# Optimization experiments

Hardware: AMD Instinct MI355X
Metric: run time of the kernel (lower is better)

## Reference

```python
import jax, jax.numpy as jnp
import numpy as np

D_MODEL = 2048
HEADS = 16
D_K = D_MODEL // HEADS  # 128
BATCH = 4
SEQ = 2048


def setup_inputs() -> dict:
    key = jax.random.key(0)
    ks = jax.random.split(key, 5)
    scale = (2.0 / (D_MODEL + D_MODEL)) ** 0.5  # trunc-normal std from init
    return {
        "x": jax.random.normal(ks[0], (BATCH, SEQ, D_MODEL), dtype=jnp.float32),
        "W_Q": jax.random.normal(ks[1], (D_MODEL, D_MODEL), dtype=jnp.float32) * scale,
        "W_K": jax.random.normal(ks[2], (D_MODEL, D_MODEL), dtype=jnp.float32) * scale,
        "W_V": jax.random.normal(ks[3], (D_MODEL, D_MODEL), dtype=jnp.float32) * scale,
        "W_O": jax.random.normal(ks[4], (D_MODEL, D_MODEL), dtype=jnp.float32) * scale,
    }


def reference(x, W_Q, W_K, W_V, W_O):
    b, s, d = x.shape
    # weights stored as [(h d_k), d_model] -> [h, d_k, d_model]
    wq = W_Q.reshape(HEADS, D_K, d)
    wk = W_K.reshape(HEADS, D_K, d)
    wv = W_V.reshape(HEADS, D_K, d)
    # projections: [b, h, s, d_k]
    Q = jnp.einsum("hkd,bsd->bhsk", wq, x)
    K = jnp.einsum("hkd,bsd->bhsk", wk, x)
    V = jnp.einsum("hvd,bsd->bhsv", wv, x)
    # causal scaled dot-product attention
    scores = jnp.einsum("bhqk,bhsk->bhqs", Q, K) / jnp.sqrt(jnp.asarray(D_K, x.dtype))
    causal = jnp.tril(jnp.ones((s, s), dtype=bool))  # True -> attend
    scores = jnp.where(causal, scores, jnp.asarray(-jnp.inf, x.dtype))
    attn = jax.nn.softmax(scores, axis=-1)
    mh = jnp.einsum("bhqs,bhsv->bhqv", attn, V)  # [b, h, s, d_v]
    # concat heads -> [b, s, h*d_v]
    mh = jnp.transpose(mh, (0, 2, 1, 3)).reshape(b, s, HEADS * D_K)
    # output projection: W_O is [d_model, (h d_v)]
    out = jnp.einsum("dm,bsm->bsd", W_O, mh)
    return out
```

## Files before the change

kernel.cpp:

```cpp
#include <hip/hip_runtime.h>
#include <stdint.h>

#define D_MODEL 2048
#define HEADS   16
#define DKH     128
#define BATCH   4
#define SEQ     2048
#define MROWS   (BATCH*SEQ)

typedef unsigned short u16;
typedef __attribute__((ext_vector_type(8))) short   short8;
typedef __attribute__((ext_vector_type(4))) float   floatx4;

#define Q_PRESCALE 0.12751744509914576f

__device__ __forceinline__ u16 f2bf(float f) {
  unsigned u = __float_as_uint(f);
  u += 0x7fffu + ((u >> 16) & 1u);
  return (u16)(u >> 16);
}
__device__ __forceinline__ u16 f2bf_fast(float f) {
  return (u16)((__float_as_uint(f) + 0x8000u) >> 16);
}

__device__ __forceinline__ void async_lds16(const u16* g, u16* l) {
  __builtin_amdgcn_global_load_lds(
      (const __attribute__((address_space(1))) unsigned int*)g,
      (__attribute__((address_space(3))) unsigned int*)l, 16, 0, 0);
}

__global__ void cast_all(const float4* __restrict__ x,  const float4* __restrict__ wq,
                         const float4* __restrict__ wk, const float4* __restrict__ wv,
                         const float4* __restrict__ wo, ushort4* __restrict__ dst) {
  int i = blockIdx.x * blockDim.x + threadIdx.x;
  int stride = gridDim.x * blockDim.x;
  for (; i < 8388608; i += stride) {
    const float4* s; int j;
    if (i < 4194304) { s = x; j = i; }
    else {
      int t = i - 4194304; int w = t >> 20; j = t & 1048575;
      s = (w == 0) ? wq : (w == 1) ? wk : (w == 2) ? wv : wo;
    }
    float4 f = s[j];
    ushort4 o;
    o.x = f2bf(f.x); o.y = f2bf(f.y); o.z = f2bf(f.z); o.w = f2bf(f.w);
    dst[i] = o;
  }
}

#define KDIM 2048
#define NKT  32

#define STAGE_A(t, buf) do { \
    const size_t go = (size_t)(t) * 64; \
    const int bo = (buf) * 32768; \
    async_lds16(sA0 + go,          dL0 + bo); \
    async_lds16(sA1 + go,          dL1 + bo); \
    async_lds16(sA0 + go + 262144, dL0 + bo + 8192); \
    async_lds16(sA1 + go + 262144, dL1 + bo + 8192); \
  } while (0)
#define STAGE_B(t, buf) do { \
    const size_t go = (size_t)(t) * 64; \
    const int bo = (buf) * 32768; \
    async_lds16(sB0 + go,          dL0 + bo + 16384); \
    async_lds16(sB1 + go,          dL1 + bo + 16384); \
    async_lds16(sB0 + go + 262144, dL0 + bo + 24576); \
    async_lds16(sB1 + go + 262144, dL1 + bo + 24576); \
  } while (0)

__device__ __forceinline__ void gemm256_core(
    const u16* __restrict__ A, const u16* __restrict__ B,
    u16* __restrict__ S, int rowBase, int colBase, floatx4 acc[8][4])
{
  const int tid  = threadIdx.x;
  const int lane = tid & 63;
  const int w    = tid >> 6;
  const int wm   = w >> 2, wn = w & 3;
  const int c    = lane & 15, quad = lane >> 4;

  const u16 *sA0, *sA1, *sB0, *sB1;
  {
    int L0 = tid * 16, L1 = 8192 + tid * 16;
    int Ls0 = L0 ^ (((L0 >> 7) & 7) << 4);
    int Ls1 = L1 ^ (((L1 >> 7) & 7) << 4);
    sA0 = A + (size_t)(rowBase + (Ls0 >> 7)) * KDIM + ((Ls0 & 127) >> 1);
    sA1 = A + (size_t)(rowBase + (Ls1 >> 7)) * KDIM + ((Ls1 & 127) >> 1);
    sB0 = B + (size_t)(colBase + (Ls0 >> 7)) * KDIM + ((Ls0 & 127) >> 1);
    sB1 = B + (size_t)(colBase + (Ls1 >> 7)) * KDIM + ((Ls1 & 127) >> 1);
  }
  u16* dL0 = S + tid * 8;
  u16* dL1 = S + 4096 + tid * 8;

  const int fo0 = (c * 128 + ((       quad * 16) ^ ((c & 7) << 4))) >> 1;
  const int fo1 = (c * 128 + ((64 +   quad * 16) ^ ((c & 7) << 4))) >> 1;
  const u16* aW = S + wm * 8192;
  const u16* bW = S + 16384 + (wn >> 1) * 8192 + (wn & 1) * 4096;

  const floatx4 z4 = {0.f, 0.f, 0.f, 0.f};
#pragma unroll
  for (int i = 0; i < 8; i++)
#pragma unroll
    for (int j = 0; j < 4; j++) acc[i][j] = z4;

  STAGE_A(0, 0); STAGE_B(0, 0);
  STAGE_A(1, 1); STAGE_B(1, 1);
  asm volatile("s_waitcnt vmcnt(8)" ::: "memory");
  __builtin_amdgcn_s_barrier();

  short8 aX[4][2], aY[4][2], bf[4][2];

#pragma unroll
  for (int i = 0; i < 4; i++) {
    aX[i][0] = *(const short8*)(aW + i * 1024 + fo0);
    aX[i][1] = *(const short8*)(aW + i * 1024 + fo1);
  }

  for (int t = 0; t < NKT; ++t) {
    const int b = t & 1;
    const u16* aB = aW + b * 32768;
    const u16* bB = bW + b * 32768;

#pragma unroll
    for (int j = 0; j < 4; j++) {
      bf[j][0] = *(const short8*)(bB + j * 1024 + fo0);
      bf[j][1] = *(const short8*)(bB + j * 1024 + fo1);
    }
#pragma unroll
    for (int i = 0; i < 4; i++) {
      aY[i][0] = *(const short8*)(aB + (4 + i) * 1024 + fo0);
      aY[i][1] = *(const short8*)(aB + (4 + i) * 1024 + fo1);
    }

    asm volatile("s_waitcnt lgkmcnt(8)" ::: "memory");
    __builtin_amdgcn_sched_barrier(0);
    __builtin_amdgcn_s_setprio(1);
#pragma unroll
    for (int i = 0; i < 4; i++)
#pragma unroll
      for (int j = 0; j < 4; j++) {
        acc[i][j] = __builtin_amdgcn_mfma_f32_16x16x32_bf16(aX[i][0], bf[j][0], acc[i][j], 0, 0, 0);
        acc[i][j] = __builtin_amdgcn_mfma_f32_16x16x32_bf16(aX[i][1], bf[j][1], acc[i][j], 0, 0, 0);
      }
    __builtin_amdgcn_s_setprio(0);

    asm volatile("s_waitcnt lgkmcnt(0)" ::: "memory");
    asm volatile("s_waitcnt vmcnt(0)" ::: "memory");
    __builtin_amdgcn_s_barrier();

    if (t + 2 < NKT) { STAGE_A(t + 2, b); STAGE_B(t + 2, b); }

    if (t + 1 < NKT) {
      const u16* aN = aW + (b ^ 1) * 32768;
#pragma unroll
      for (int i = 0; i < 4; i++) {
        aX[i][0] = *(const short8*)(aN + i * 1024 + fo0);
        aX[i][1] = *(const short8*)(aN + i * 1024 + fo1);
      }
    }
    __builtin_amdgcn_sched_barrier(0);
    __builtin_amdgcn_s_setprio(1);
#pragma unroll
    for (int i = 0; i < 4; i++)
#pragma unroll
      for (int j = 0; j < 4; j++) {
        acc[4 + i][j] = __builtin_amdgcn_mfma_f32_16x16x32_bf16(aY[i][0], bf[j][0], acc[4 + i][j], 0, 0, 0);
        acc[4 + i][j] = __builtin_amdgcn_mfma_f32_16x16x32_bf16(aY[i][1], bf[j][1], acc[4 + i][j], 0, 0, 0);
      }
    __builtin_amdgcn_s_setprio(0);
  }
}

__global__ __launch_bounds__(512, 2) void gemm_qkv(
    const u16* __restrict__ A, const u16* __restrict__ B,
    u16* __restrict__ Qb, u16* __restrict__ Kb, u16* __restrict__ Vpb)
{
  __shared__ __align__(16) u16 S[65536];

  const int tid  = threadIdx.x;
  const int lane = tid & 63;
  const int w    = tid >> 6;
  const int wm   = w >> 2, wn = w & 3;
  const int c    = lane & 15, quad = lane >> 4;
  const int rowBase = blockIdx.x * 256;
  const int colBase = blockIdx.y * 256;

  floatx4 acc[8][4];
  gemm256_core(A, B, S, rowBase, colBase, acc);

  const int proj = colBase >> 11;
  const float esc = (proj == 0) ? Q_PRESCALE : 1.0f;
  u16* dst = (proj == 0) ? Qb : (proj == 1) ? Kb : Vpb;

#pragma unroll
  for (int i = 0; i < 8; i++) {
#pragma unroll
    for (int j = 0; j < 4; j++) {
#pragma unroll
      for (int r = 0; r < 4; r++) {
        int row = rowBase + wm * 128 + i * 16 + quad * 4 + r;
        int col = (colBase & 2047) + wn * 64 + j * 16 + c;
        float v = acc[i][j][r] * esc;
        if (proj < 2) {
          size_t idx = ((size_t)((row >> 11) * HEADS + (col >> 7)) * SEQ + (row & 2047)) * DKH + (col & 127);
          dst[idx] = f2bf(v);
        } else {
          int srow = row & 2047;
          int sp = (srow & ~127) | (((srow & 15) << 3) | ((srow >> 4) & 7));
          size_t idx = ((size_t)((row >> 11) * HEADS + (col >> 7)) * DKH + (col & 127)) * SEQ + sp;
          dst[idx] = f2bf(v);
        }
      }
    }
  }
}

__global__ __launch_bounds__(512, 2) void gemm_out(
    const u16* __restrict__ A, const u16* __restrict__ B,
    float* __restrict__ Cout)
{
  __shared__ __align__(16) u16 S[65536];

  const int tid  = threadIdx.x;
  const int lane = tid & 63;
  const int w    = tid >> 6;
  const int wm   = w >> 2, wn = w & 3;
  const int c    = lane & 15, quad = lane >> 4;
  const int rowBase = blockIdx.x * 256;
  const int colBase = blockIdx.y * 256;

  floatx4 acc[8][4];
  gemm256_core(A, B, S, rowBase, colBase, acc);

#pragma unroll
  for (int i = 0; i < 8; i++)
#pragma unroll
    for (int j = 0; j < 4; j++)
#pragma unroll
      for (int r = 0; r < 4; r++) {
        int row = rowBase + wm * 128 + i * 16 + quad * 4 + r;
        int col = colBase + wn * 64 + j * 16 + c;
        Cout[(size_t)row * D_MODEL + col] = acc[i][j][r];
      }
}

__global__ __launch_bounds__(256, 1) void attn_fwd(
    const u16* __restrict__ Qg, const u16* __restrict__ Kg,
    const u16* __restrict__ Vpg, u16* __restrict__ mh)
{
  __shared__ __align__(16) u16 Sh[2 * 16384 + 16384 + 4 * 32 * 136];

  const int tid  = threadIdx.x;
  const int lane = tid & 63;
  const int w    = tid >> 6;
  const int c    = lane & 15, quad = lane >> 4;
  const int bh   = blockIdx.x;
  const int qt   = 15 - blockIdx.y;
  const int q0   = qt * 128;

  const u16* Qbh = Qg  + (size_t)bh * SEQ * DKH;
  const u16* Kbh = Kg  + (size_t)bh * SEQ * DKH;
  const u16* Vbh = Vpg + (size_t)bh * DKH * SEQ;

  u16* Vs = Sh + 32768;
  u16* Pw = Sh + 49152 + w * 32 * 136;

  const int rowb = tid >> 4;
  const int cbh  = (((tid & 15) ^ (rowb & 7)) << 3);
  const u16* sK = Kbh + rowb * DKH + cbh;
  const u16* sV = Vbh + (size_t)rowb * SEQ + cbh;

  int fof[4];
#pragma unroll
  for (int ks = 0; ks < 4; ks++)
    fof[ks] = ((ks * 64 + quad * 16) ^ ((c & 7) << 4)) >> 1;

#define STAGE_K_ATTN(kbN, buf) do { \
    u16* d_ = Sh + (buf) * 16384 + tid * 8; \
    const u16* s_ = sK + (size_t)(kbN) * DKH; \
    _Pragma("unroll") \
    for (int q_ = 0; q_ < 8; q_++) async_lds16(s_ + q_ * 2048, d_ + q_ * 2048); \
  } while (0)
#define STAGE_V_ATTN(kb_) do { \
    u16* d_ = Vs + tid * 8; \
    const u16* s_ = sV + (kb_); \
    _Pragma("unroll") \
    for (int q_ = 0; q_ < 8; q_++) async_lds16(s_ + (size_t)q_ * 16 * SEQ, d_ + q_ * 2048); \
  } while (0)

  short8 qf[2][4];
#pragma unroll
  for (int m2 = 0; m2 < 2; m2++)
#pragma unroll
    for (int ks = 0; ks < 4; ks++)
      qf[m2][ks] = *(const short8*)&Qbh[(size_t)(q0 + w * 32 + m2 * 16 + c) * DKH + ks * 32 + quad * 8];

  const floatx4 z4 = {0.f, 0.f, 0.f, 0.f};
  floatx4 oacc[2][8];
#pragma unroll
  for (int m2 = 0; m2 < 2; m2++)
#pragma unroll
    for (int d = 0; d < 8; d++) oacc[m2][d] = z4;
  float lrow[2][4];
#pragma unroll
  for (int m2 = 0; m2 < 2; m2++)
#pragma unroll
    for (int r = 0; r < 4; r++) lrow[m2][r] = 0.f;

  STAGE_K_ATTN(0, 0);
  __syncthreads();

  for (int kt = 0; kt <= qt; kt++) {
    const int kb = kt * 128;
    const u16* Kc = Sh + (kt & 1) * 16384;

    STAGE_V_ATTN(kb);
    if (kt < qt) STAGE_K_ATTN(kb + 128, (kt + 1) & 1);

    short8 kf[4][8];
#pragma unroll
    for (int ks = 0; ks < 4; ks++)
#pragma unroll
      for (int n = 0; n < 8; n++)
        kf[ks][n] = *(const short8*)&Kc[(n * 16 + c) * 128 + fof[ks]];

    floatx4 s[2][8];
#pragma unroll
    for (int m2 = 0; m2 < 2; m2++)
#pragma unroll
      for (int n = 0; n < 8; n++) s[m2][n] = z4;
#pragma unroll
    for (int ks = 0; ks < 4; ks++)
#pragma unroll
      for (int n = 0; n < 8; n++) {
        s[0][n] = __builtin_amdgcn_mfma_f32_16x16x32_bf16(qf[0][ks], kf[ks][n], s[0][n], 0, 0, 0);
        s[1][n] = __builtin_amdgcn_mfma_f32_16x16x32_bf16(qf[1][ks], kf[ks][n], s[1][n], 0, 0, 0);
      }

    if (kt == qt) {
#pragma unroll
      for (int m2 = 0; m2 < 2; m2++)
#pragma unroll
        for (int n = 0; n < 8; n++)
#pragma unroll
          for (int r = 0; r < 4; r++) {
            int qrow = w * 32 + m2 * 16 + quad * 4 + r;
            int key  = n * 16 + c;
            if (key > qrow) s[m2][n][r] = -3.0e38f;
          }
    }

#pragma unroll
    for (int m2 = 0; m2 < 2; m2++) {
#pragma unroll
      for (int r = 0; r < 4; r++) {
        float rs = 0.f;
#pragma unroll
        for (int n = 0; n < 8; n++) {
          float p = __builtin_amdgcn_exp2f(s[m2][n][r]);
          s[m2][n][r] = p;
          rs += p;
        }
        rs += __shfl_xor(rs, 1);
        rs += __shfl_xor(rs, 2);
        rs += __shfl_xor(rs, 4);
        rs += __shfl_xor(rs, 8);
        lrow[m2][r] += rs;
      }
    }

#pragma unroll
    for (int m2 = 0; m2 < 2; m2++) {
#pragma unroll
      for (int r = 0; r < 4; r++) {
        short8 pk;
#pragma unroll
        for (int n = 0; n < 8; n++) pk[n] = (short)f2bf_fast(s[m2][n][r]);
        *(short8*)&Pw[(m2 * 16 + quad * 4 + r) * 136 + c * 8] = pk;
      }
    }
    short8 pf[2][4];
#pragma unroll
    for (int m2 = 0; m2 < 2; m2++)
#pragma unroll
      for (int ks = 0; ks < 4; ks++)
        pf[m2][ks] = *(const short8*)&Pw[(m2 * 16 + c) * 136 + ks * 32 + quad * 8];

    __syncthreads();

    short8 vf[8][4];
#pragma unroll
    for (int d = 0; d < 8; d++)
#pragma unroll
      for (int ks = 0; ks < 4; ks++)
        vf[d][ks] = *(const short8*)&Vs[(d * 16 + c) * 128 + fof[ks]];

#pragma unroll
    for (int d = 0; d < 8; d++)
#pragma unroll
      for (int ks = 0; ks < 4; ks++) {
        oacc[0][d] = __builtin_amdgcn_mfma_f32_16x16x32_bf16(pf[0][ks], vf[d][ks], oacc[0][d], 0, 0, 0);
        oacc[1][d] = __builtin_amdgcn_mfma_f32_16x16x32_bf16(pf[1][ks], vf[d][ks], oacc[1][d], 0, 0, 0);
      }

    __syncthreads();
  }

  const int b = bh >> 4, h = bh & 15;
#pragma unroll
  for (int m2 = 0; m2 < 2; m2++) {
#pragma unroll
    for (int r = 0; r < 4; r++) {
      float rl = 1.0f / lrow[m2][r];
      int qrow = q0 + w * 32 + m2 * 16 + quad * 4 + r;
      u16* dst = mh + ((size_t)(b * SEQ + qrow)) * D_MODEL + h * DKH;
#pragma unroll
      for (int d = 0; d < 8; d++)
        dst[d * 16 + c] = f2bf(oacc[m2][d][r] * rl);
    }
  }
}

extern "C" void kernel_launch(void* const* d_in, const int* in_sizes, int n_in,
                              void* d_out, int out_size, void* d_ws, size_t ws_size,
                              hipStream_t stream) {
  const float* x  = (const float*)d_in[0];
  const float* wq = (const float*)d_in[1];
  const float* wk = (const float*)d_in[2];
  const float* wv = (const float*)d_in[3];
  const float* wo = (const float*)d_in[4];
  float* out = (float*)d_out;

  u16* ws  = (u16*)d_ws;
  u16* xb  = ws;
  u16* wqb = xb  + 16777216;
  u16* wkb = wqb + 4194304;
  u16* wvb = wkb + 4194304;
  u16* wob = wvb + 4194304;
  u16* Qb  = wob + 4194304;
  u16* Kb  = Qb  + 16777216;
  u16* Vpb = Kb  + 16777216;
  u16* mhb = Vpb + 16777216;

  cast_all<<<4096, 256, 0, stream>>>((const float4*)x,  (const float4*)wq,
                                     (const float4*)wk, (const float4*)wv,
                                     (const float4*)wo, (ushort4*)xb);

  gemm_qkv<<<dim3(32, 24), 512, 0, stream>>>(xb, wqb, Qb, Kb, Vpb);

  attn_fwd<<<dim3(64, 16), 256, 0, stream>>>(Qb, Kb, Vpb, mhb);

  gemm_out<<<dim3(32, 8), 512, 0, stream>>>(mhb, wob, out);
}
```

Before: 586.7 us.

## Halve attention key tile to raise occupancy, add XCD-aware GEMM block swizzle

The attention kernel now processes keys in 64-wide tiles instead of 128. LDS use and the register footprint both shrink, so two blocks can share a CU, and the V layout permutation is changed to match the smaller tile. Barriers are replaced with explicit vmcnt waits, letting the next K tile's load stay in flight while V is consumed. Both GEMMs remap block indices so consecutive tiles land on the same XCD for L2 reuse. The cost is twice as many loop iterations and barriers per query tile.

```diff
diff --git a/kernel.cpp b/kernel.cpp
--- a/kernel.cpp
+++ b/kernel.cpp
@@ -10,6 +10,7 @@
 
 typedef unsigned short u16;
 typedef __attribute__((ext_vector_type(8))) short   short8;
+typedef __attribute__((ext_vector_type(4))) short   short4v;
 typedef __attribute__((ext_vector_type(4))) float   floatx4;
 
 #define Q_PRESCALE 0.12751744509914576f
@@ -170,6 +171,13 @@
   }
 }
 
+__device__ __forceinline__ int xcd_swz_flat() {
+  int nx = gridDim.x;
+  int flat = blockIdx.y * nx + blockIdx.x;
+  int cpx = (nx * gridDim.y) >> 3;
+  return (flat & 7) * cpx + (flat >> 3);
+}
+
 __global__ __launch_bounds__(512, 2) void gemm_qkv(
     const u16* __restrict__ A, const u16* __restrict__ B,
     u16* __restrict__ Qb, u16* __restrict__ Kb, u16* __restrict__ Vpb)
@@ -181,8 +189,9 @@
   const int w    = tid >> 6;
   const int wm   = w >> 2, wn = w & 3;
   const int c    = lane & 15, quad = lane >> 4;
-  const int rowBase = blockIdx.x * 256;
-  const int colBase = blockIdx.y * 256;
+  const int swz  = xcd_swz_flat();
+  const int rowBase = (swz & 31) * 256;
+  const int colBase = (swz >> 5) * 256;
 
   floatx4 acc[8][4];
   gemm256_core(A, B, S, rowBase, colBase, acc);
@@ -205,7 +214,7 @@
           dst[idx] = f2bf(v);
         } else {
           int srow = row & 2047;
-          int sp = (srow & ~127) | (((srow & 15) << 3) | ((srow >> 4) & 7));
+          int sp = (srow & ~63) | (((srow & 15) << 2) | ((srow >> 4) & 3));
           size_t idx = ((size_t)((row >> 11) * HEADS + (col >> 7)) * DKH + (col & 127)) * SEQ + sp;
           dst[idx] = f2bf(v);
         }
@@ -225,8 +234,9 @@
   const int w    = tid >> 6;
   const int wm   = w >> 2, wn = w & 3;
   const int c    = lane & 15, quad = lane >> 4;
-  const int rowBase = blockIdx.x * 256;
-  const int colBase = blockIdx.y * 256;
+  const int swz  = xcd_swz_flat();
+  const int rowBase = (swz & 31) * 256;
+  const int colBase = (swz >> 5) * 256;
 
   floatx4 acc[8][4];
   gemm256_core(A, B, S, rowBase, colBase, acc);
@@ -243,11 +253,11 @@
       }
 }
 
-__global__ __launch_bounds__(256, 1) void attn_fwd(
+__global__ __launch_bounds__(256, 2) void attn_fwd(
     const u16* __restrict__ Qg, const u16* __restrict__ Kg,
     const u16* __restrict__ Vpg, u16* __restrict__ mh)
 {
-  __shared__ __align__(16) u16 Sh[2 * 16384 + 16384 + 4 * 32 * 136];
+  __shared__ __align__(16) u16 Sh[2 * 8192 + 8192 + 4 * 32 * 72];
 
   const int tid  = threadIdx.x;
   const int lane = tid & 63;
@@ -256,35 +266,36 @@
   const int bh   = blockIdx.x;
   const int qt   = 15 - blockIdx.y;
   const int q0   = qt * 128;
+  const int nkt  = 2 * qt + 2;
 
   const u16* Qbh = Qg  + (size_t)bh * SEQ * DKH;
   const u16* Kbh = Kg  + (size_t)bh * SEQ * DKH;
   const u16* Vbh = Vpg + (size_t)bh * DKH * SEQ;
 
-  u16* Vs = Sh + 32768;
-  u16* Pw = Sh + 49152 + w * 32 * 136;
-
-  const int rowb = tid >> 4;
-  const int cbh  = (((tid & 15) ^ (rowb & 7)) << 3);
-  const u16* sK = Kbh + rowb * DKH + cbh;
-  const u16* sV = Vbh + (size_t)rowb * SEQ + cbh;
+  u16* Vs = Sh + 16384;
+  u16* Pw = Sh + 24576 + w * 32 * 72;
+
+  const int rowK = tid >> 4;
+  const u16* sK  = Kbh + rowK * DKH + (((tid & 15) ^ (rowK & 7)) << 3);
+  const int rowV = tid >> 3;
+  const u16* sV  = Vbh + (size_t)rowV * SEQ + (((tid & 7) ^ (rowV & 7)) << 3);
 
   int fof[4];
 #pragma unroll
   for (int ks = 0; ks < 4; ks++)
     fof[ks] = ((ks * 64 + quad * 16) ^ ((c & 7) << 4)) >> 1;
 
-#define STAGE_K_ATTN(kbN, buf) do { \
-    u16* d_ = Sh + (buf) * 16384 + tid * 8; \
+#define STAGE_K64(kbN, buf) do { \
+    u16* d_ = Sh + (buf) * 8192 + tid * 8; \
     const u16* s_ = sK + (size_t)(kbN) * DKH; \
     _Pragma("unroll") \
-    for (int q_ = 0; q_ < 8; q_++) async_lds16(s_ + q_ * 2048, d_ + q_ * 2048); \
+    for (int q_ = 0; q_ < 4; q_++) async_lds16(s_ + q_ * (16 * DKH), d_ + q_ * 2048); \
   } while (0)
-#define STAGE_V_ATTN(kb_) do { \
+#define STAGE_V64(kb_) do { \
     u16* d_ = Vs + tid * 8; \
     const u16* s_ = sV + (kb_); \
     _Pragma("unroll") \
-    for (int q_ = 0; q_ < 8; q_++) async_lds16(s_ + (size_t)q_ * 16 * SEQ, d_ + q_ * 2048); \
+    for (int q_ = 0; q_ < 4; q_++) async_lds16(s_ + (size_t)q_ * (32 * SEQ), d_ + q_ * 2048); \
   } while (0)
 
   short8 qf[2][4];
@@ -306,45 +317,46 @@
 #pragma unroll
     for (int r = 0; r < 4; r++) lrow[m2][r] = 0.f;
 
-  STAGE_K_ATTN(0, 0);
-  __syncthreads();
-
-  for (int kt = 0; kt <= qt; kt++) {
-    const int kb = kt * 128;
-    const u16* Kc = Sh + (kt & 1) * 16384;
-
-    STAGE_V_ATTN(kb);
-    if (kt < qt) STAGE_K_ATTN(kb + 128, (kt + 1) & 1);
-
-    short8 kf[4][8];
+  STAGE_K64(0, 0);
+  asm volatile("s_waitcnt vmcnt(0)" ::: "memory");
+  __builtin_amdgcn_s_barrier();
+
+  for (int kt = 0; kt < nkt; kt++) {
+    const int kb = kt * 64;
+    const u16* Kc = Sh + (kt & 1) * 8192;
+
+    STAGE_V64(kb);
+    if (kt + 1 < nkt) STAGE_K64(kb + 64, (kt + 1) & 1);
+
+    short8 kf[4][4];
 #pragma unroll
     for (int ks = 0; ks < 4; ks++)
 #pragma unroll
-      for (int n = 0; n < 8; n++)
+      for (int n = 0; n < 4; n++)
         kf[ks][n] = *(const short8*)&Kc[(n * 16 + c) * 128 + fof[ks]];
 
-    floatx4 s[2][8];
+    floatx4 s[2][4];
 #pragma unroll
     for (int m2 = 0; m2 < 2; m2++)
 #pragma unroll
-      for (int n = 0; n < 8; n++) s[m2][n] = z4;
+      for (int n = 0; n < 4; n++) s[m2][n] = z4;
 #pragma unroll
     for (int ks = 0; ks < 4; ks++)
 #pragma unroll
-      for (int n = 0; n < 8; n++) {
+      for (int n = 0; n < 4; n++) {
         s[0][n] = __builtin_amdgcn_mfma_f32_16x16x32_bf16(qf[0][ks], kf[ks][n], s[0][n], 0, 0, 0);
         s[1][n] = __builtin_amdgcn_mfma_f32_16x16x32_bf16(qf[1][ks], kf[ks][n], s[1][n], 0, 0, 0);
       }
 
-    if (kt == qt) {
+    if (kt >= nkt - 2) {
 #pragma unroll
       for (int m2 = 0; m2 < 2; m2++)
 #pragma unroll
-        for (int n = 0; n < 8; n++)
+        for (int n = 0; n < 4; n++)
 #pragma unroll
           for (int r = 0; r < 4; r++) {
-            int qrow = w * 32 + m2 * 16 + quad * 4 + r;
-            int key  = n * 16 + c;
+            int qrow = q0 + w * 32 + m2 * 16 + quad * 4 + r;
+            int key  = kb + n * 16 + c;
             if (key > qrow) s[m2][n][r] = -3.0e38f;
           }
     }
@@ -355,7 +367,7 @@
       for (int r = 0; r < 4; r++) {
         float rs = 0.f;
 #pragma unroll
-        for (int n = 0; n < 8; n++) {
+        for (int n = 0; n < 4; n++) {
           float p = __builtin_amdgcn_exp2f(s[m2][n][r]);
           s[m2][n][r] = p;
           rs += p;
@@ -372,37 +384,42 @@
     for (int m2 = 0; m2 < 2; m2++) {
 #pragma unroll
       for (int r = 0; r < 4; r++) {
-        short8 pk;
-#pragma unroll
-        for (int n = 0; n < 8; n++) pk[n] = (short)f2bf_fast(s[m2][n][r]);
-        *(short8*)&Pw[(m2 * 16 + quad * 4 + r) * 136 + c * 8] = pk;
-      }
-    }
-    short8 pf[2][4];
+        short4v pk;
+#pragma unroll
+        for (int n = 0; n < 4; n++) pk[n] = (short)f2bf_fast(s[m2][n][r]);
+        *(short4v*)&Pw[(m2 * 16 + quad * 4 + r) * 72 + c * 4] = pk;
+      }
+    }
+    short8 pf[2][2];
 #pragma unroll
     for (int m2 = 0; m2 < 2; m2++)
 #pragma unroll
-      for (int ks = 0; ks < 4; ks++)
-        pf[m2][ks] = *(const short8*)&Pw[(m2 * 16 + c) * 136 + ks * 32 + quad * 8];
-
-    __syncthreads();
-
-    short8 vf[8][4];
+      for (int ks = 0; ks < 2; ks++)
+        pf[m2][ks] = *(const short8*)&Pw[(m2 * 16 + c) * 72 + ks * 32 + quad * 8];
+
+    if (kt + 1 < nkt) asm volatile("s_waitcnt vmcnt(4)" ::: "memory");
+    else              asm volatile("s_waitcnt vmcnt(0)" ::: "memory");
+    __builtin_amdgcn_s_barrier();
+
+    short8 vf[8][2];
 #pragma unroll
     for (int d = 0; d < 8; d++)
 #pragma unroll
-      for (int ks = 0; ks < 4; ks++)
-        vf[d][ks] = *(const short8*)&Vs[(d * 16 + c) * 128 + fof[ks]];
+      for (int ks = 0; ks < 2; ks++)
+        vf[d][ks] = *(const short8*)&Vs[(d * 16 + c) * 64 + fof[ks]];
 
 #pragma unroll
     for (int d = 0; d < 8; d++)
 #pragma unroll
-      for (int ks = 0; ks < 4; ks++) {
+      for (int ks = 0; ks < 2; ks++) {
         oacc[0][d] = __builtin_amdgcn_mfma_f32_16x16x32_bf16(pf[0][ks], vf[d][ks], oacc[0][d], 0, 0, 0);
         oacc[1][d] = __builtin_amdgcn_mfma_f32_16x16x32_bf16(pf[1][ks], vf[d][ks], oacc[1][d], 0, 0, 0);
       }
 
-    __syncthreads();
+    if (kt + 1 < nkt) {
+      asm volatile("s_waitcnt vmcnt(0)" ::: "memory");
+      __builtin_amdgcn_s_barrier();
+    }
   }
 
   const int b = bh >> 4, h = bh & 15;
```

Measured after the change: 596.2 us. Within noise of the previous version (+1.6%).
